# Kernel tuning notes

Hardware: AMD Instinct MI355X
Metric: run time of the kernel (lower is better)

The kernel has to match this reference:

```python
import jax, jax.numpy as jnp
import numpy as np

D_MODEL = 1024
NUM_HEADS = 16
MAX_LEN = 512  # chunk_size
BATCH = 2
SEQ_LEN = 2048


def _mha(x, w_in, b_in, w_out, b_out, num_heads):
    """torch.nn.MultiheadAttention (eval mode, self-attn) over the last-but-one axis.
    x: (..., S, d). Packed in-proj weight w_in: (3d, d), out-proj w_out: (d, d)."""
    *batch, S, d = x.shape
    hd = d // num_heads
    qkv = x @ w_in.T + b_in                      # (..., S, 3d)
    q, k, v = jnp.split(qkv, 3, axis=-1)
    def heads(t):
        return t.reshape(*batch, S, num_heads, hd)
    q, k, v = heads(q), heads(k), heads(v)
    scale = 1.0 / np.sqrt(hd).astype(np.float32)
    scores = jnp.einsum('...qhd,...khd->...hqk', q, k) * scale
    attn = jax.nn.softmax(scores, axis=-1)
    o = jnp.einsum('...hqk,...khd->...qhd', attn, v).reshape(*batch, S, d)
    return o @ w_out.T + b_out


def setup_inputs() -> dict:
    key = jax.random.key(0)
    ks = jax.random.split(key, 5)
    d = D_MODEL
    s = 0.02
    return {
        'x': jax.random.normal(ks[0], (BATCH, SEQ_LEN, d), dtype=jnp.float32),
        'w_in_l': jax.random.normal(ks[1], (3 * d, d), dtype=jnp.float32) * s,
        'b_in_l': jnp.zeros((3 * d,), jnp.float32),
        'w_out_l': jax.random.normal(ks[2], (d, d), dtype=jnp.float32) * s,
        'b_out_l': jnp.zeros((d,), jnp.float32),
        'w_in_g': jax.random.normal(ks[3], (3 * d, d), dtype=jnp.float32) * s,
        'b_in_g': jnp.zeros((3 * d,), jnp.float32),
        'w_out_g': jax.random.normal(ks[4], (d, d), dtype=jnp.float32) * s,
        'b_out_g': jnp.zeros((d,), jnp.float32),
    }


def reference(x, w_in_l, b_in_l, w_out_l, b_out_l, w_in_g, b_in_g, w_out_g, b_out_g):
    B, S, d = x.shape
    cs = MAX_LEN
    nc = S // cs
    # (B, nc, cs, d) -> (B, cs, nc, d): for each intra-chunk position, attend across chunks.
    xc = x.reshape(B, nc, cs, d).transpose(0, 2, 1, 3)
    # Vectorized replacement for the python loop over chunk positions:
    # batched MHA with batch (B, cs) and sequence length nc.
    loc = _mha(xc, w_in_l, b_in_l, w_out_l, b_out_l, NUM_HEADS)  # (B, cs, nc, d)
    # Faithful to torch: stack -> (nc, cs, B, d), transpose(1,2) -> (nc, B, cs, d),
    # then raw reshape to (B, S, d) (a layout-reinterpreting view, preserved here).
    loc = loc.transpose(2, 0, 1, 3).reshape(B, S, d)
    # Global full self-attention over the whole sequence.
    return _mha(loc, w_in_g, b_in_g, w_out_g, b_out_g, NUM_HEADS)
```

## Files before the change

### kernel.cpp

```cpp
#include <hip/hip_runtime.h>

#define BB 2
#define SS 2048
#define DD 1024
#define HH 16
#define HD 64
#define CS 512
#define NC 4
#define TD 3072
#define MM 4096

typedef __attribute__((ext_vector_type(8))) short short8;
typedef __attribute__((ext_vector_type(4))) float floatx4;

__device__ __forceinline__ float bf2f(unsigned short h) {
  union { unsigned int u; float f; } v; v.u = ((unsigned int)h) << 16; return v.f;
}
__device__ __forceinline__ unsigned short f2bf(float f) {
  union { float f; unsigned int u; } v; v.f = f;
  unsigned int r = (v.u + 0x7fffu + ((v.u >> 16) & 1u)) >> 16;
  return (unsigned short)r;
}
__device__ __forceinline__ short8 ld8f(const float* p) {
  floatx4 f0 = *(const floatx4*)p;
  floatx4 f1 = *(const floatx4*)(p + 4);
  short8 o;
  o[0] = (short)f2bf(f0[0]); o[1] = (short)f2bf(f0[1]);
  o[2] = (short)f2bf(f0[2]); o[3] = (short)f2bf(f0[3]);
  o[4] = (short)f2bf(f1[0]); o[5] = (short)f2bf(f1[1]);
  o[6] = (short)f2bf(f1[2]); o[7] = (short)f2bf(f1[3]);
  return o;
}
__device__ __forceinline__ short8 scale8_eighth(short8 a) {
  short8 o;
#pragma unroll
  for (int j = 0; j < 8; ++j) o[j] = (short)f2bf(bf2f((unsigned short)a[j]) * 0.125f);
  return o;
}
__device__ __forceinline__ void async16(const void* g, void* l) {
  __builtin_amdgcn_global_load_lds((const __attribute__((address_space(1))) void*)g,
                                   (__attribute__((address_space(3))) void*)l, 16, 0, 0);
}

__global__ __launch_bounds__(256) void cvt_all(
    const float* __restrict__ s0, unsigned short* __restrict__ d0, int n0,
    const float* __restrict__ s1, unsigned short* __restrict__ d1, int n1,
    const float* __restrict__ s2, unsigned short* __restrict__ d2, int n2,
    const float* __restrict__ s3, unsigned short* __restrict__ d3, int n3) {
  int bb = blockIdx.x;
  const float* s; unsigned short* d; int off;
  if (bb < n0) { s = s0; d = d0; off = bb; }
  else if (bb < n0 + n1) { s = s1; d = d1; off = bb - n0; }
  else if (bb < n0 + n1 + n2) { s = s2; d = d2; off = bb - n0 - n1; }
  else { s = s3; d = d3; off = bb - n0 - n1 - n2; }
  int i = (off * 256 + threadIdx.x) * 8;
  *(short8*)(d + i) = ld8f(s + i);
}

__global__ __launch_bounds__(256) void cvt_bf16(const float* __restrict__ in,
                                                unsigned short* __restrict__ out, int n) {
  int i = (blockIdx.x * 256 + threadIdx.x) * 8;
  if (i < n) *(short8*)(out + i) = ld8f(in + i);
}

template <int MT, int C_F32>
__global__ __launch_bounds__(256) void gemm_bt_bias(
    const unsigned short* __restrict__ A, const unsigned short* __restrict__ W,
    const float* __restrict__ bias, void* __restrict__ Cv, int M, int N, int K) {
  constexpr int AI = MT / 32;
  __shared__ unsigned short sA[MT * 32];
  __shared__ unsigned short sB[128 * 32];
  const int tid = threadIdx.x;
  const int wid = tid >> 6, lane = tid & 63;
  const int quad = lane >> 4, l15 = lane & 15;
  const int wm = wid & 1, wn = wid >> 1;
  const int bm = blockIdx.y, bn = blockIdx.x;

  floatx4 acc[AI][4];
#pragma unroll
  for (int i = 0; i < AI; ++i)
#pragma unroll
    for (int j = 0; j < 4; ++j) acc[i][j] = (floatx4){0.f, 0.f, 0.f, 0.f};

  const int r = tid >> 2;
  const int kc = (tid & 3) * 8;
  const unsigned short* gA = A + (size_t)(bm * MT + r) * K + kc;
  const unsigned short* gW = W + (size_t)(bn * 128 + r) * K + kc;
  unsigned short* lA = sA + wid * 512;
  unsigned short* lB = sB + wid * 512;

  for (int k0 = 0; k0 < K; k0 += 32) {
#pragma unroll
    for (int s = 0; s < MT / 64; ++s)
      async16(gA + (size_t)(s * 64) * K + k0, lA + s * 2048);
    async16(gW + k0, lB);
    async16(gW + (size_t)64 * K + k0, lB + 2048);
    __syncthreads();

    short8 af[AI], bfr[4];
#pragma unroll
    for (int i = 0; i < AI; ++i)
      af[i] = *(const short8*)(sA + (wm * (MT / 2) + i * 16 + l15) * 32 + quad * 8);
#pragma unroll
    for (int j = 0; j < 4; ++j)
      bfr[j] = *(const short8*)(sB + (wn * 64 + j * 16 + l15) * 32 + quad * 8);
#pragma unroll
    for (int i = 0; i < AI; ++i)
#pragma unroll
      for (int j = 0; j < 4; ++j)
        acc[i][j] = __builtin_amdgcn_mfma_f32_16x16x32_bf16(af[i], bfr[j], acc[i][j], 0, 0, 0);
    __syncthreads();
  }

#pragma unroll
  for (int j = 0; j < 4; ++j) {
    int n = bn * 128 + wn * 64 + j * 16 + l15;
    float bv = bias[n];
#pragma unroll
    for (int i = 0; i < AI; ++i) {
      int mrow = bm * MT + wm * (MT / 2) + i * 16 + quad * 4;
#pragma unroll
      for (int rr = 0; rr < 4; ++rr) {
        float v = acc[i][j][rr] + bv;
        if (C_F32) ((float*)Cv)[(size_t)(mrow + rr) * N + n] = v;
        else ((unsigned short*)Cv)[(size_t)(mrow + rr) * N + n] = f2bf(v);
      }
    }
  }
}

__global__ __launch_bounds__(256) void attn_local(const unsigned short* __restrict__ QKV,
                                                  unsigned short* __restrict__ O) {
  const int tid = threadIdx.x;
  const int wid = tid >> 6, lane = tid & 63;
  const int idx = blockIdx.x * 4 + wid;
  const int h = idx & 15, c = (idx >> 4) & 511, b = idx >> 13;

  float q[NC], k[NC], v[NC];
#pragma unroll
  for (int n = 0; n < NC; ++n) {
    size_t base = (size_t)(b * SS + n * CS + c) * TD + h * HD + lane;
    q[n] = bf2f(QKV[base]);
    k[n] = bf2f(QKV[base + DD]);
    v[n] = bf2f(QKV[base + 2 * DD]);
  }
  float s[NC][NC];
#pragma unroll
  for (int m = 0; m < NC; ++m)
#pragma unroll
    for (int n = 0; n < NC; ++n) {
      float p = q[m] * k[n];
#pragma unroll
      for (int off = 32; off >= 1; off >>= 1) p += __shfl_xor(p, off);
      s[m][n] = p * 0.125f;
    }
#pragma unroll
  for (int m = 0; m < NC; ++m) {
    float mx = fmaxf(fmaxf(s[m][0], s[m][1]), fmaxf(s[m][2], s[m][3]));
    float e[NC], sum = 0.f;
#pragma unroll
    for (int n = 0; n < NC; ++n) { e[n] = __expf(s[m][n] - mx); sum += e[n]; }
    float o = (e[0] * v[0] + e[1] * v[1] + e[2] * v[2] + e[3] * v[3]) / sum;
    O[(size_t)(m * (BB * CS) + b * CS + c) * DD + h * HD + lane] = f2bf(o);
  }
}

__global__ __launch_bounds__(256) void transpose_v(const unsigned short* __restrict__ QKV,
                                                   unsigned short* __restrict__ VT) {
  __shared__ unsigned short sT[64 * 64];
  const int tid = threadIdx.x;
  const int bh = blockIdx.x, b = bh >> 4, h = bh & 15;
  const int s0 = blockIdx.y * 64;
#pragma unroll
  for (int it = 0; it < 2; ++it) {
    int C = it * 256 + tid;
    int t = C >> 3, dc = C & 7;
    short8 v = *(const short8*)(QKV + (size_t)(b * SS + s0 + t) * TD + 2 * DD + h * HD + dc * 8);
    *(short8*)(sT + t * 64 + ((dc ^ (t & 7)) << 3)) = v;
  }
  __syncthreads();
#pragma unroll
  for (int it = 0; it < 2; ++it) {
    int C = it * 256 + tid;
    int d = C >> 3, tc = C & 7;
    short8 o;
#pragma unroll
    for (int j = 0; j < 8; ++j) {
      int t = tc * 8 + j;
      o[j] = (short)sT[t * 64 + (((d >> 3) ^ (t & 7)) << 3) + (d & 7)];
    }
    *(short8*)(VT + ((size_t)(bh * 64 + d)) * SS + s0 + tc * 8) = o;
  }
}

__global__ __launch_bounds__(256) void attn_global(
    const unsigned short* __restrict__ Q, const unsigned short* __restrict__ Kp,
    const unsigned short* __restrict__ VT, unsigned short* __restrict__ O) {
  __shared__ unsigned short sK[2][64 * 64];
  __shared__ unsigned short sVT[2][64 * 64];
  __shared__ unsigned short sP[4][32 * 64];
  __shared__ float lsumBuf[64];
  const int tid = threadIdx.x;
  const int wid = tid >> 6, lane = tid & 63;
  const int quad = lane >> 4, l15 = lane & 15;
  const int qhalf = wid & 1, khalf = wid >> 1;
  const int bh = blockIdx.x;
  const int b = bh >> 4, h = bh & 15;
  const int q0 = blockIdx.y * 64 + qhalf * 32;

  short8 qf[2][2];
#pragma unroll
  for (int g = 0; g < 2; ++g) {
    const unsigned short* qr = Q + (size_t)(b * SS + q0 + g * 16 + l15) * TD + h * HD + quad * 8;
    qf[g][0] = scale8_eighth(*(const short8*)qr);
    qf[g][1] = scale8_eighth(*(const short8*)(qr + 32));
  }

  float lsum[2][4];
  floatx4 oacc[2][4];
#pragma unroll
  for (int g = 0; g < 2; ++g)
#pragma unroll
    for (int s = 0; s < 4; ++s) { lsum[g][s] = 0.f; oacc[g][s] = (floatx4){0.f, 0.f, 0.f, 0.f}; }

  unsigned short* myP = &sP[wid][0];
  const unsigned short* myK = &sK[khalf][0];
  const unsigned short* myV = &sVT[khalf][0];
  const unsigned short* vbase = VT + (size_t)(bh * 64) * SS;

  for (int t = 0; t < 16; ++t) {
#pragma unroll
    for (int kh = 0; kh < 2; ++kh) {
      const int kbase = (kh * 16 + t) * 64;
#pragma unroll
      for (int it = 0; it < 2; ++it) {
        int P = it * 256 + tid;
        int key = P >> 3, dc = P & 7;
        short8 kv = *(const short8*)(Kp + (size_t)(b * SS + kbase + key) * TD + h * HD + dc * 8);
        *(short8*)(&sK[kh][0] + key * 64 + ((dc ^ (key & 7)) << 3)) = kv;
      }
#pragma unroll
      for (int it = 0; it < 2; ++it) {
        int P = it * 256 + tid;
        int dim = P >> 3, kcc = P & 7;
        short8 vv = *(const short8*)(vbase + (size_t)dim * SS + kbase + kcc * 8);
        *(short8*)(&sVT[kh][0] + dim * 64 + ((kcc ^ (dim & 7)) << 3)) = vv;
      }
    }
    __syncthreads();

    floatx4 sacc[2][4];
#pragma unroll
    for (int sub = 0; sub < 4; ++sub) {
      int key = sub * 16 + l15;
      int c0 = (quad ^ (key & 7)) << 3;
      short8 kf0 = *(const short8*)(myK + key * 64 + c0);
      short8 kf1 = *(const short8*)(myK + key * 64 + (c0 ^ 32));
#pragma unroll
      for (int g = 0; g < 2; ++g) {
        floatx4 z = (floatx4){0.f, 0.f, 0.f, 0.f};
        z = __builtin_amdgcn_mfma_f32_16x16x32_bf16(qf[g][0], kf0, z, 0, 0, 0);
        z = __builtin_amdgcn_mfma_f32_16x16x32_bf16(qf[g][1], kf1, z, 0, 0, 0);
        sacc[g][sub] = z;
      }
    }

#pragma unroll
    for (int g = 0; g < 2; ++g)
#pragma unroll
      for (int sub = 0; sub < 4; ++sub) {
        int kc8 = sub * 2 + (l15 >> 3), k7 = l15 & 7;
#pragma unroll
        for (int rr = 0; rr < 4; ++rr) {
          unsigned int u = __float_as_uint(__expf(sacc[g][sub][rr]));
          lsum[g][rr] += __uint_as_float(u & 0xffff0000u);
          int row = g * 16 + quad * 4 + rr;
          myP[row * 64 + ((kc8 ^ (row & 7)) << 3) + k7] = (unsigned short)(u >> 16);
        }
      }
    __asm__ volatile("s_waitcnt lgkmcnt(0)" ::: "memory");

    short8 pf[2][2];
#pragma unroll
    for (int g = 0; g < 2; ++g) {
      int row = g * 16 + l15;
      int sw = row & 7;
#pragma unroll
      for (int c = 0; c < 2; ++c)
        pf[g][c] = *(const short8*)(myP + row * 64 + (((c * 4 + quad) ^ sw) << 3));
    }

#pragma unroll
    for (int sub = 0; sub < 4; ++sub) {
      int n = sub * 16 + l15;
      int v0 = (quad ^ (n & 7)) << 3;
      short8 vt0 = *(const short8*)(myV + n * 64 + v0);
      short8 vt1 = *(const short8*)(myV + n * 64 + (v0 ^ 32));
#pragma unroll
      for (int g = 0; g < 2; ++g) {
        oacc[g][sub] = __builtin_amdgcn_mfma_f32_16x16x32_bf16(pf[g][0], vt0, oacc[g][sub], 0, 0, 0);
        oacc[g][sub] = __builtin_amdgcn_mfma_f32_16x16x32_bf16(pf[g][1], vt1, oacc[g][sub], 0, 0, 0);
      }
    }
    __syncthreads();
  }

  float lred[2][4];
#pragma unroll
  for (int g = 0; g < 2; ++g)
#pragma unroll
    for (int rr = 0; rr < 4; ++rr) {
      float t = lsum[g][rr];
#pragma unroll
      for (int off = 8; off >= 1; off >>= 1) t += __shfl_xor(t, off);
      lred[g][rr] = t;
    }

  float* obuf = (float*)&sP[0][0];
  if (khalf == 1) {
    float* my = obuf + qhalf * 2048;
#pragma unroll
    for (int g = 0; g < 2; ++g)
#pragma unroll
      for (int sub = 0; sub < 4; ++sub)
#pragma unroll
        for (int rr = 0; rr < 4; ++rr)
          my[(g * 16 + quad * 4 + rr) * 64 + sub * 16 + l15] = oacc[g][sub][rr];
    if (l15 == 0)
#pragma unroll
      for (int g = 0; g < 2; ++g)
#pragma unroll
        for (int rr = 0; rr < 4; ++rr)
          lsumBuf[qhalf * 32 + g * 16 + quad * 4 + rr] = lred[g][rr];
  }
  __syncthreads();
  if (khalf == 0) {
    float* my = obuf + qhalf * 2048;
#pragma unroll
    for (int g = 0; g < 2; ++g) {
#pragma unroll
      for (int rr = 0; rr < 4; ++rr)
        lred[g][rr] = 1.f / (lred[g][rr] + lsumBuf[qhalf * 32 + g * 16 + quad * 4 + rr]);
#pragma unroll
      for (int sub = 0; sub < 4; ++sub)
#pragma unroll
        for (int rr = 0; rr < 4; ++rr) {
          float v = oacc[g][sub][rr] + my[(g * 16 + quad * 4 + rr) * 64 + sub * 16 + l15];
          int row = b * SS + q0 + g * 16 + quad * 4 + rr;
          O[(size_t)row * DD + h * HD + sub * 16 + l15] = f2bf(v * lred[g][rr]);
        }
    }
  }
}

extern "C" void kernel_launch(void* const* d_in, const int* in_sizes, int n_in,
                              void* d_out, int out_size, void* d_ws, size_t ws_size,
                              hipStream_t stream) {
  const float* x       = (const float*)d_in[0];
  const float* w_in_l  = (const float*)d_in[1];
  const float* b_in_l  = (const float*)d_in[2];
  const float* w_out_l = (const float*)d_in[3];
  const float* b_out_l = (const float*)d_in[4];
  const float* w_in_g  = (const float*)d_in[5];
  const float* b_in_g  = (const float*)d_in[6];
  const float* w_out_g = (const float*)d_in[7];
  const float* b_out_g = (const float*)d_in[8];

  unsigned short* wsA = (unsigned short*)d_ws;
  unsigned short* wsB = wsA + (size_t)MM * TD;
  unsigned short* dob = (unsigned short*)d_out;
  unsigned short* wbf_out_l = dob;
  unsigned short* wbf_in_g  = dob + (size_t)DD * DD;
  unsigned short* wbf_in_l  = dob + 4 * (size_t)DD * DD;
  unsigned short* o1        = dob + 4 * (size_t)DD * DD;
  unsigned short* vtbuf     = dob;

  dim3 blk(256);
  cvt_all<<<dim3(5632), blk, 0, stream>>>(w_out_l, wbf_out_l, 512,
                                          w_in_g, wbf_in_g, 1536,
                                          w_in_l, wbf_in_l, 1536,
                                          x, wsB, 2048);

  gemm_bt_bias<128, 0><<<dim3(TD / 128, MM / 128), blk, 0, stream>>>(wsB, wbf_in_l, b_in_l, wsA, MM, TD, DD);
  attn_local<<<dim3(BB * CS * HH / 4), blk, 0, stream>>>(wsA, o1);
  gemm_bt_bias<64, 0><<<dim3(DD / 128, MM / 64), blk, 0, stream>>>(o1, wbf_out_l, b_out_l, wsB, MM, DD, DD);
  gemm_bt_bias<128, 0><<<dim3(TD / 128, MM / 128), blk, 0, stream>>>(wsB, wbf_in_g, b_in_g, wsA, MM, TD, DD);
  transpose_v<<<dim3(BB * HH, SS / 64), blk, 0, stream>>>(wsA, vtbuf);
  attn_global<<<dim3(BB * HH, SS / 64), blk, 0, stream>>>(wsA, wsA + DD, vtbuf, wsB);
  cvt_bf16<<<dim3(DD * DD / 2048), blk, 0, stream>>>(w_out_g, wsA, DD * DD);
  gemm_bt_bias<64, 1><<<dim3(DD / 128, MM / 64), blk, 0, stream>>>(wsB, wsA, b_out_g, d_out, MM, DD, DD);
}
```

Baseline: 332.7 us.

## Prefetch next K/V tile into registers during attention compute in global attention

The global attention kernel now issues the global loads for the next K and V^T tile into registers before computing on the current tile, then writes them to shared memory after the compute finishes. The aim is to hide global memory latency behind the MFMA and softmax work. It also raises MFMA wave priority with s_setprio and sets a minimum occupancy of 3 blocks in launch bounds. The cost is extra registers for the prefetch buffers, an added barrier per iteration, and possible spills under the tighter register limit.

```diff
diff --git a/kernel.cpp b/kernel.cpp
--- a/kernel.cpp
+++ b/kernel.cpp
@@ -193,7 +193,7 @@
   }
 }
 
-__global__ __launch_bounds__(256) void attn_global(
+__global__ __launch_bounds__(256, 3) void attn_global(
     const unsigned short* __restrict__ Q, const unsigned short* __restrict__ Kp,
     const unsigned short* __restrict__ VT, unsigned short* __restrict__ O) {
   __shared__ unsigned short sK[2][64 * 64];
@@ -228,28 +228,40 @@
   const unsigned short* myV = &sVT[khalf][0];
   const unsigned short* vbase = VT + (size_t)(bh * 64) * SS;
 
+  const unsigned short* gK[4]; unsigned short* lK[4];
+  const unsigned short* gV[4]; unsigned short* lV[4];
+#pragma unroll
+  for (int kh = 0; kh < 2; ++kh)
+#pragma unroll
+    for (int it = 0; it < 2; ++it) {
+      const int j = kh * 2 + it;
+      const int P = it * 256 + tid;
+      const int row = P >> 3, c8 = P & 7;
+      gK[j] = Kp + (size_t)(b * SS + kh * 1024 + row) * TD + h * HD + c8 * 8;
+      lK[j] = &sK[kh][0] + row * 64 + ((c8 ^ (row & 7)) << 3);
+      gV[j] = vbase + (size_t)row * SS + kh * 1024 + c8 * 8;
+      lV[j] = &sVT[kh][0] + row * 64 + ((c8 ^ (row & 7)) << 3);
+    }
+
+  short8 rK[4], rV[4];
+#pragma unroll
+  for (int j = 0; j < 4; ++j) { rK[j] = *(const short8*)gK[j]; rV[j] = *(const short8*)gV[j]; }
+#pragma unroll
+  for (int j = 0; j < 4; ++j) { *(short8*)lK[j] = rK[j]; *(short8*)lV[j] = rV[j]; }
+  __syncthreads();
+
   for (int t = 0; t < 16; ++t) {
-#pragma unroll
-    for (int kh = 0; kh < 2; ++kh) {
-      const int kbase = (kh * 16 + t) * 64;
-#pragma unroll
-      for (int it = 0; it < 2; ++it) {
-        int P = it * 256 + tid;
-        int key = P >> 3, dc = P & 7;
-        short8 kv = *(const short8*)(Kp + (size_t)(b * SS + kbase + key) * TD + h * HD + dc * 8);
-        *(short8*)(&sK[kh][0] + key * 64 + ((dc ^ (key & 7)) << 3)) = kv;
+    if (t < 15) {
+#pragma unroll
+      for (int j = 0; j < 4; ++j) {
+        rK[j] = *(const short8*)(gK[j] + (size_t)(t + 1) * (64 * TD));
+        rV[j] = *(const short8*)(gV[j] + (t + 1) * 64);
       }
-#pragma unroll
-      for (int it = 0; it < 2; ++it) {
-        int P = it * 256 + tid;
-        int dim = P >> 3, kcc = P & 7;
-        short8 vv = *(const short8*)(vbase + (size_t)dim * SS + kbase + kcc * 8);
-        *(short8*)(&sVT[kh][0] + dim * 64 + ((kcc ^ (dim & 7)) << 3)) = vv;
-      }
-    }
-    __syncthreads();
+    }
+    __builtin_amdgcn_sched_barrier(0);
 
     floatx4 sacc[2][4];
+    __builtin_amdgcn_s_setprio(1);
 #pragma unroll
     for (int sub = 0; sub < 4; ++sub) {
       int key = sub * 16 + l15;
@@ -264,6 +276,7 @@
         sacc[g][sub] = z;
       }
     }
+    __builtin_amdgcn_s_setprio(0);
 
 #pragma unroll
     for (int g = 0; g < 2; ++g)
@@ -290,6 +303,7 @@
         pf[g][c] = *(const short8*)(myP + row * 64 + (((c * 4 + quad) ^ sw) << 3));
     }
 
+    __builtin_amdgcn_s_setprio(1);
 #pragma unroll
     for (int sub = 0; sub < 4; ++sub) {
       int n = sub * 16 + l15;
@@ -301,6 +315,13 @@
         oacc[g][sub] = __builtin_amdgcn_mfma_f32_16x16x32_bf16(pf[g][0], vt0, oacc[g][sub], 0, 0, 0);
         oacc[g][sub] = __builtin_amdgcn_mfma_f32_16x16x32_bf16(pf[g][1], vt1, oacc[g][sub], 0, 0, 0);
       }
+    }
+    __builtin_amdgcn_s_setprio(0);
+    __syncthreads();
+
+    if (t < 15) {
+#pragma unroll
+      for (int j = 0; j < 4; ++j) { *(short8*)lK[j] = rK[j]; *(short8*)lV[j] = rV[j]; }
     }
     __syncthreads();
   }
```

Result: slower. 360.0 us (+8.2%).

## Double GEMM K-tile to 64 with XOR-swizzled LDS layout

Applied to the files above, without the earlier changes.

The bf16 GEMM now loads a K-slab of 64 per iteration instead of 32, halving the number of barrier pairs per K loop and doing two MFMA sub-steps per slab. The shared-memory tile is stored with an XOR swizzle of the 16-byte column chunk by row, meant to avoid LDS bank conflicts on the fragment reads. The cost is doubled LDS usage per block, which may reduce occupancy, and the loads remain unpipelined.

```diff
diff --git a/kernel.cpp b/kernel.cpp
--- a/kernel.cpp
+++ b/kernel.cpp
@@ -68,8 +68,8 @@
     const unsigned short* __restrict__ A, const unsigned short* __restrict__ W,
     const float* __restrict__ bias, void* __restrict__ Cv, int M, int N, int K) {
   constexpr int AI = MT / 32;
-  __shared__ unsigned short sA[MT * 32];
-  __shared__ unsigned short sB[128 * 32];
+  __shared__ unsigned short sA[MT * 64];
+  __shared__ unsigned short sB[128 * 64];
   const int tid = threadIdx.x;
   const int wid = tid >> 6, lane = tid & 63;
   const int quad = lane >> 4, l15 = lane & 15;
@@ -82,33 +82,41 @@
 #pragma unroll
     for (int j = 0; j < 4; ++j) acc[i][j] = (floatx4){0.f, 0.f, 0.f, 0.f};
 
-  const int r = tid >> 2;
-  const int kc = (tid & 3) * 8;
-  const unsigned short* gA = A + (size_t)(bm * MT + r) * K + kc;
-  const unsigned short* gW = W + (size_t)(bn * 128 + r) * K + kc;
+  const int rb = tid >> 3;
+  const int colsw = ((tid & 7) ^ (rb & 7)) << 3;
+  const unsigned short* gA = A + (size_t)(bm * MT + rb) * K + colsw;
+  const unsigned short* gW = W + (size_t)(bn * 128 + rb) * K + colsw;
   unsigned short* lA = sA + wid * 512;
   unsigned short* lB = sB + wid * 512;
 
-  for (int k0 = 0; k0 < K; k0 += 32) {
-#pragma unroll
-    for (int s = 0; s < MT / 64; ++s)
-      async16(gA + (size_t)(s * 64) * K + k0, lA + s * 2048);
-    async16(gW + k0, lB);
-    async16(gW + (size_t)64 * K + k0, lB + 2048);
+  for (int k0 = 0; k0 < K; k0 += 64) {
+#pragma unroll
+    for (int i = 0; i < MT / 32; ++i)
+      async16(gA + (size_t)(i * 32) * K + k0, lA + i * 2048);
+#pragma unroll
+    for (int i = 0; i < 4; ++i)
+      async16(gW + (size_t)(i * 32) * K + k0, lB + i * 2048);
     __syncthreads();
 
-    short8 af[AI], bfr[4];
-#pragma unroll
-    for (int i = 0; i < AI; ++i)
-      af[i] = *(const short8*)(sA + (wm * (MT / 2) + i * 16 + l15) * 32 + quad * 8);
-#pragma unroll
-    for (int j = 0; j < 4; ++j)
-      bfr[j] = *(const short8*)(sB + (wn * 64 + j * 16 + l15) * 32 + quad * 8);
-#pragma unroll
-    for (int i = 0; i < AI; ++i)
-#pragma unroll
-      for (int j = 0; j < 4; ++j)
-        acc[i][j] = __builtin_amdgcn_mfma_f32_16x16x32_bf16(af[i], bfr[j], acc[i][j], 0, 0, 0);
+#pragma unroll
+    for (int kk = 0; kk < 2; ++kk) {
+      short8 af[AI], bfr[4];
+#pragma unroll
+      for (int i = 0; i < AI; ++i) {
+        int row = wm * (MT / 2) + i * 16 + l15;
+        af[i] = *(const short8*)(sA + row * 64 + ((((kk << 2) | quad) ^ (row & 7)) << 3));
+      }
+#pragma unroll
+      for (int j = 0; j < 4; ++j) {
+        int row = wn * 64 + j * 16 + l15;
+        bfr[j] = *(const short8*)(sB + row * 64 + ((((kk << 2) | quad) ^ (row & 7)) << 3));
+      }
+#pragma unroll
+      for (int i = 0; i < AI; ++i)
+#pragma unroll
+        for (int j = 0; j < 4; ++j)
+          acc[i][j] = __builtin_amdgcn_mfma_f32_16x16x32_bf16(af[i], bfr[j], acc[i][j], 0, 0, 0);
+    }
     __syncthreads();
   }
 
```

Result: faster. 324.3 us (-2.5%).
